# Kernel tuning notes

Measured on AMD Instinct MI355X. Metric: run time of the kernel, lower is better.

Reference implementation:

```python
import jax, jax.numpy as jnp
import numpy as np
from jax import lax

DS = 4  # downsample_factor

def setup_inputs() -> dict:
    key = jax.random.key(0)
    ks = jax.random.split(key, 7)
    B, C, H, W = 4, 256, 256, 256
    Cq = C // 16  # reduction=16
    return {
        "x":  jax.random.normal(ks[0], (B, C, H, W), dtype=jnp.float32),
        "Wq": jax.random.normal(ks[1], (Cq, C), dtype=jnp.float32) * 0.05,
        "bq": jax.random.normal(ks[2], (Cq,), dtype=jnp.float32) * 0.05,
        "Wk": jax.random.normal(ks[3], (Cq, C), dtype=jnp.float32) * 0.05,
        "bk": jax.random.normal(ks[4], (Cq,), dtype=jnp.float32) * 0.05,
        "Wv": jax.random.normal(ks[5], (C, C), dtype=jnp.float32) * 0.05,
        "bv": jax.random.normal(ks[6], (C,), dtype=jnp.float32) * 0.05,
    }

def reference(x, Wq, bq, Wk, bk, Wv, bv):
    B, C, H, W = x.shape
    # MaxPool2d(kernel=DS, stride=DS)
    xd = lax.reduce_window(x, -jnp.inf, lax.max,
                           (1, 1, DS, DS), (1, 1, DS, DS), 'VALID')
    h, w = xd.shape[2], xd.shape[3]
    N = h * w
    # 1x1 convs == channel-wise linear maps
    q = jnp.einsum('oc,bchw->bohw', Wq, xd) + bq[None, :, None, None]
    k = jnp.einsum('oc,bchw->bohw', Wk, xd) + bk[None, :, None, None]
    v = jnp.einsum('oc,bchw->bohw', Wv, xd) + bv[None, :, None, None]
    query = q.reshape(B, -1, N).transpose(0, 2, 1)   # [B, N, Cq]
    key_  = k.reshape(B, -1, N)                      # [B, Cq, N]
    value = v.reshape(B, C, N).transpose(0, 2, 1)    # [B, N, C]
    att = jnp.einsum('bnc,bcm->bnm', query, key_)    # [B, N, N]
    # global-mean threshold masking (zeros, not -inf, per original)
    att = jnp.where(att < att.mean(), 0.0, att)
    att = jax.nn.softmax(att, axis=-1)
    out = jnp.einsum('bnm,bmc->bnc', att, value)     # [B, N, C]
    out = out.transpose(0, 2, 1).reshape(B, C, h, w)
    # bilinear upsample, align_corners=False (half-pixel centers)
    out = jax.image.resize(out, (B, C, H, W), method='bilinear')
    return out + x
```

## Files before the change

kernel.cpp:

```cpp
#include <hip/hip_runtime.h>
#include <hip/hip_bf16.h>
#include <cmath>
#include <cstdint>
#include <cstddef>

typedef unsigned short u16;
typedef __attribute__((ext_vector_type(8))) __bf16 bf16x8;
typedef __attribute__((ext_vector_type(4))) float f32x4;
typedef __attribute__((ext_vector_type(8))) unsigned short us8;
typedef __attribute__((ext_vector_type(4))) unsigned short us4;

static const size_t OFF_XD32  = 0;
static const size_t OFF_QT    = 16777216;
static const size_t OFF_KT    = 17825792;
static const size_t OFF_VT    = 18874368;
static const size_t OFF_WF    = 27262976;
static const size_t OFF_SPART = 27394048;

__device__ __forceinline__ void gl2lds16(const void* gsrc, void* ldst) {
  __builtin_amdgcn_global_load_lds(
      (const __attribute__((address_space(1))) unsigned int*)gsrc,
      (__attribute__((address_space(3))) unsigned int*)ldst, 16, 0, 0);
}

__device__ __forceinline__ float hmax4(float4 v) {
  return fmaxf(fmaxf(v.x, v.y), fmaxf(v.z, v.w));
}

__global__ __launch_bounds__(256) void k_pre(const float* __restrict__ x,
                                             const float* __restrict__ Wv,
                                             float* __restrict__ xd32,
                                             u16* __restrict__ Wf) {
  const int tid = threadIdx.x;
  if (blockIdx.x < 16) {
    const int rt = blockIdx.x;
#pragma unroll
    for (int i = 0; i < 2; ++i) {
      int s = tid + i * 256;
      int ks = s >> 6, lane = s & 63;
      const float* src = Wv + (size_t)(rt * 16 + (lane & 15)) * 256u + ks * 32 + (lane >> 4) * 8;
      float4 a = *reinterpret_cast<const float4*>(src);
      float4 b = *reinterpret_cast<const float4*>(src + 4);
      us8 o;
      o[0] = __builtin_bit_cast(u16, __float2bfloat16(a.x));
      o[1] = __builtin_bit_cast(u16, __float2bfloat16(a.y));
      o[2] = __builtin_bit_cast(u16, __float2bfloat16(a.z));
      o[3] = __builtin_bit_cast(u16, __float2bfloat16(a.w));
      o[4] = __builtin_bit_cast(u16, __float2bfloat16(b.x));
      o[5] = __builtin_bit_cast(u16, __float2bfloat16(b.y));
      o[6] = __builtin_bit_cast(u16, __float2bfloat16(b.z));
      o[7] = __builtin_bit_cast(u16, __float2bfloat16(b.w));
      *reinterpret_cast<us8*>(Wf + ((size_t)((rt * 8 + ks) * 64 + lane)) * 8u) = o;
    }
  } else {
    unsigned idx = (blockIdx.x - 16) * 256u + tid;
    unsigned xo = idx & 63u;
    unsigned yo = (idx >> 6) & 63u;
    unsigned bc = idx >> 12;
    const float* base = x + (size_t)bc * 65536u + yo * 1024u + xo * 4u;
    float m = -1e30f;
#pragma unroll
    for (int dy = 0; dy < 4; ++dy) {
      float4 v = *reinterpret_cast<const float4*>(base + dy * 256);
      m = fmaxf(m, hmax4(v));
    }
    xd32[(size_t)bc * 4096u + yo * 64u + xo] = m;
  }
}

__global__ __launch_bounds__(512) void k_qkv(const float* __restrict__ xd32,
                                             const u16* __restrict__ Wf, const float* __restrict__ bv,
                                             const float* __restrict__ Wq, const float* __restrict__ bq,
                                             const float* __restrict__ Wk, const float* __restrict__ bk,
                                             float* __restrict__ qT, float* __restrict__ kT,
                                             u16* __restrict__ vT, float* __restrict__ Spart) {
  __shared__ char smem[65536];
  const int tid = threadIdx.x;

  if (blockIdx.x < 256) {
    u16 (*Bf)[8][64][8] = reinterpret_cast<u16(*)[8][64][8]>(smem);
    const int blk = blockIdx.x;
    const int b = blk >> 6, n0 = (blk & 63) * 64;
    const int w = tid >> 6, lane = tid & 63;

#pragma unroll
    for (int p = 0; p < 8; ++p) {
      int idx = p * 512 + tid;
      int k = idx >> 4, q4 = idx & 15;
      float4 v = *reinterpret_cast<const float4*>(
          xd32 + ((size_t)b * 256 + k) * 4096u + n0 + q4 * 4);
      int ks = k >> 5, kl = (k >> 3) & 3, j = k & 7;
      int ct = q4 >> 2, nb = (q4 & 3) * 4;
      Bf[ct][ks][kl * 16 + nb + 0][j] = __builtin_bit_cast(u16, __float2bfloat16(v.x));
      Bf[ct][ks][kl * 16 + nb + 1][j] = __builtin_bit_cast(u16, __float2bfloat16(v.y));
      Bf[ct][ks][kl * 16 + nb + 2][j] = __builtin_bit_cast(u16, __float2bfloat16(v.z));
      Bf[ct][ks][kl * 16 + nb + 3][j] = __builtin_bit_cast(u16, __float2bfloat16(v.w));
    }
    __syncthreads();

    f32x4 acc[2][4];
#pragma unroll
    for (int r = 0; r < 2; ++r)
#pragma unroll
      for (int ct = 0; ct < 4; ++ct) acc[r][ct] = (f32x4){0.f, 0.f, 0.f, 0.f};
    __builtin_amdgcn_s_setprio(1);
    for (int ks = 0; ks < 8; ++ks) {
      bf16x8 Bv[4];
#pragma unroll
      for (int ct = 0; ct < 4; ++ct)
        Bv[ct] = __builtin_bit_cast(bf16x8, *reinterpret_cast<const us8*>(&Bf[ct][ks][lane][0]));
#pragma unroll
      for (int r = 0; r < 2; ++r) {
        int rt = w * 2 + r;
        bf16x8 Av = __builtin_bit_cast(bf16x8,
            *reinterpret_cast<const us8*>(Wf + ((size_t)((rt * 8 + ks) * 64 + lane)) * 8u));
#pragma unroll
        for (int ct = 0; ct < 4; ++ct)
          acc[r][ct] = __builtin_amdgcn_mfma_f32_16x16x32_bf16(Av, Bv[ct], acc[r][ct], 0, 0, 0);
      }
    }
    __builtin_amdgcn_s_setprio(0);

#pragma unroll
    for (int r = 0; r < 2; ++r) {
      int row0 = (w * 2 + r) * 16 + (lane >> 4) * 4;
#pragma unroll
      for (int rr = 0; rr < 4; ++rr) {
        int c = row0 + rr;
        float bb = bv[c];
        u16* dst = vT + ((size_t)b * 256 + c) * 4096u + n0 + (lane & 15);
#pragma unroll
        for (int ct = 0; ct < 4; ++ct)
          dst[ct * 16] = __builtin_bit_cast(u16, __float2bfloat16(acc[r][ct][rr] + bb));
      }
    }
  } else {
    float (*xs)[64] = reinterpret_cast<float(*)[64]>(smem);
    const int qb = blockIdx.x - 256;
    const int b = qb >> 6, n0 = (qb & 63) * 64;
    {
      const float* src = xd32 + (size_t)b * 1048576u + n0;
#pragma unroll
      for (int i = 0; i < 8; ++i) {
        int slot = tid + i * 512;
        int c = slot >> 4, q4 = slot & 15;
        *reinterpret_cast<float4*>(&xs[c][q4 * 4]) =
            *reinterpret_cast<const float4*>(src + (size_t)c * 4096u + q4 * 4);
      }
    }
    __syncthreads();
    const int o = tid >> 4, t4 = tid & 15;
    const float* wrow = (o < 16) ? (Wq + (size_t)o * 256u) : (Wk + (size_t)(o - 16) * 256u);
    float a0 = 0.f, a1 = 0.f, a2 = 0.f, a3 = 0.f;
    for (int c = 0; c < 256; ++c) {
      float w = wrow[c];
      float4 xv = *reinterpret_cast<const float4*>(&xs[c][t4 * 4]);
      a0 = fmaf(w, xv.x, a0);
      a1 = fmaf(w, xv.y, a1);
      a2 = fmaf(w, xv.z, a2);
      a3 = fmaf(w, xv.w, a3);
    }
    float* dst = (o < 16) ? qT : kT;
    int oo = (o < 16) ? o : (o - 16);
    float bb = (o < 16) ? bq[oo] : bk[oo];
    size_t base = ((size_t)b * 4096u + n0 + t4 * 4) * 16u + oo;
    dst[base]      = a0 + bb;
    dst[base + 16] = a1 + bb;
    dst[base + 32] = a2 + bb;
    dst[base + 48] = a3 + bb;
    float s = a0 + a1 + a2 + a3;
    s += __shfl_xor(s, 1); s += __shfl_xor(s, 2);
    s += __shfl_xor(s, 4); s += __shfl_xor(s, 8);
    if (t4 == 0) Spart[(size_t)qb * 32u + o] = s;
  }
}

__global__ __launch_bounds__(512) void k_flash(const float* __restrict__ qT,
                                               const float* __restrict__ kT,
                                               const u16* __restrict__ vT,
                                               const float* __restrict__ Spart,
                                               const float* __restrict__ bq,
                                               const float* __restrict__ bk,
                                               float* __restrict__ ods) {
  __shared__ u16 vbuf[2][16384];
  __shared__ u16 kfh[2][4][64][8];
  __shared__ u16 kfl[2][4][64][8];
  __shared__ u16 pfr[8][2][64][8];
  __shared__ float mean_s;

  const int orig = blockIdx.x;
  const int b    = (orig >> 1) & 3;
  const int row0 = (((orig & 1) << 5) | (orig >> 3)) * 64;
  const int tid  = threadIdx.x;
  const int w    = tid >> 6;
  const int lane = tid & 63;
  const int wq   = w & 3;
  const int wc   = w >> 2;
  const int g    = lane >> 4;
  const int c16  = lane & 15;

  if (tid < 64) {
    int bb = tid >> 4, o = tid & 15;
    float sq = 4096.0f * bq[o], sk = 4096.0f * bk[o];
    for (int s = 0; s < 64; ++s) {
      const float* p = Spart + ((size_t)(bb * 64 + s)) * 32u;
      sq += p[o];
      sk += p[16 + o];
    }
    float pr = sq * sk;
#pragma unroll
    for (int off = 32; off > 0; off >>= 1) pr += __shfl_down(pr, off);
    if (tid == 0) mean_s = pr * (1.0f / 67108864.0f);
  }

  float qv[16];
  {
    const float* qrow = qT + ((size_t)b*4096 + row0 + 16*wq + c16) * 16;
#pragma unroll
    for (int i = 0; i < 4; ++i) {
      float4 t4 = reinterpret_cast<const float4*>(qrow)[i];
      qv[4*i] = t4.x; qv[4*i+1] = t4.y; qv[4*i+2] = t4.z; qv[4*i+3] = t4.w;
    }
  }
  u16 qhi[16], qlo[16];
#pragma unroll
  for (int i = 0; i < 16; ++i) {
    __hip_bfloat16 h = __float2bfloat16(qv[i]);
    float fh = __bfloat162float(h);
    __hip_bfloat16 lo = __float2bfloat16(qv[i] - fh);
    qhi[i] = __builtin_bit_cast(u16, h);
    qlo[i] = __builtin_bit_cast(u16, lo);
  }
  us8 a1u, a2u;
  {
    const bool koff8  = (g & 1);
    const bool lo_src = (g >= 2);
#pragma unroll
    for (int i = 0; i < 8; ++i) {
      u16 hs = koff8 ? qhi[i+8] : qhi[i];
      u16 ls = koff8 ? qlo[i+8] : qlo[i];
      a1u[i] = lo_src ? ls : hs;
      a2u[i] = lo_src ? (u16)0 : hs;
    }
  }
  const bf16x8 A1 = __builtin_bit_cast(bf16x8, a1u);
  const bf16x8 A2 = __builtin_bit_cast(bf16x8, a2u);

  f32x4 O[8];
#pragma unroll
  for (int i = 0; i < 8; ++i) O[i] = (f32x4){0.f, 0.f, 0.f, 0.f};
  float Lr[4] = {0.f, 0.f, 0.f, 0.f};
  float M = 0.0f;

  const int kv_s = tid >> 2, t4v = tid & 3;
  const int ks = kv_s >> 4, kld0 = (kv_s & 15) + 16*(t4v >> 1), ki0 = 4*(t4v & 1);

  {
    const u16* vsrc = vT + (size_t)b*256*4096;
#pragma unroll
    for (int i = 0; i < 4; ++i) {
      int u = i*512 + tid;
      int row = u >> 3, slot = u & 7;
      int sb = (slot*16) ^ ((row & 7) << 4);
      gl2lds16((const char*)(vsrc + (size_t)row*4096) + sb, (char*)&vbuf[0][0] + u*16);
    }
    if (tid < 256) {
      float4 kvec = *reinterpret_cast<const float4*>(kT + ((size_t)b*4096 + kv_s)*16 + 4*t4v);
      float kf[4] = {kvec.x, kvec.y, kvec.z, kvec.w};
      us4 h4, l4;
#pragma unroll
      for (int di = 0; di < 4; ++di) {
        __hip_bfloat16 h = __float2bfloat16(kf[di]);
        float fh = __bfloat162float(h);
        __hip_bfloat16 lo = __float2bfloat16(kf[di] - fh);
        h4[di] = __builtin_bit_cast(u16, h);
        l4[di] = __builtin_bit_cast(u16, lo);
      }
      *reinterpret_cast<us4*>(&kfh[0][ks][kld0][ki0])    = h4;
      *reinterpret_cast<us4*>(&kfh[0][ks][kld0+32][ki0]) = h4;
      *reinterpret_cast<us4*>(&kfl[0][ks][kld0][ki0])    = l4;
      *reinterpret_cast<us4*>(&kfl[0][ks][kld0+32][ki0]) = l4;
    }
  }
  __syncthreads();
  const float mean = mean_s;

  for (int t = 0; t < 64; ++t) {
    const int cur = t & 1, nxt = cur ^ 1;
    const int kv0n = ((t + 1) & 63) * 64;

    float4 kvec;
    if (tid < 256)
      kvec = *reinterpret_cast<const float4*>(kT + ((size_t)b*4096 + kv0n + kv_s)*16 + 4*t4v);
    {
      const u16* vsrc = vT + (size_t)b*256*4096 + kv0n;
#pragma unroll
      for (int i = 0; i < 4; ++i) {
        int u = i*512 + tid;
        int row = u >> 3, slot = u & 7;
        int sb = (slot*16) ^ ((row & 7) << 4);
        gl2lds16((const char*)(vsrc + (size_t)row*4096) + sb, (char*)&vbuf[nxt][0] + u*16);
      }
    }

    f32x4 S[4];
    __builtin_amdgcn_s_setprio(1);
#pragma unroll
    for (int s = 0; s < 4; ++s) {
      bf16x8 bh = __builtin_bit_cast(bf16x8, *reinterpret_cast<const us8*>(&kfh[cur][s][lane][0]));
      bf16x8 bl = __builtin_bit_cast(bf16x8, *reinterpret_cast<const us8*>(&kfl[cur][s][lane][0]));
      f32x4 acc = (f32x4){0.f, 0.f, 0.f, 0.f};
      acc = __builtin_amdgcn_mfma_f32_16x16x32_bf16(A1, bh, acc, 0, 0, 0);
      acc = __builtin_amdgcn_mfma_f32_16x16x32_bf16(A2, bl, acc, 0, 0, 0);
      S[s] = acc;
    }
    __builtin_amdgcn_s_setprio(0);

    float pmax = -1e30f;
#pragma unroll
    for (int s = 0; s < 4; ++s)
#pragma unroll
      for (int r = 0; r < 4; ++r) {
        float v = S[s][r];
        v = (v < mean) ? 0.f : v;
        S[s][r] = v;
        pmax = fmaxf(pmax, v);
      }
    if (!__all(pmax <= M + 8.0f)) {
      float mw = pmax;
#pragma unroll
      for (int off = 1; off < 64; off <<= 1) mw = fmaxf(mw, __shfl_xor(mw, off));
      float Mn = fmaxf(M, mw);
      float sc = __expf(M - Mn);
#pragma unroll
      for (int i = 0; i < 8; ++i) {
        O[i][0] *= sc; O[i][1] *= sc; O[i][2] *= sc; O[i][3] *= sc;
      }
#pragma unroll
      for (int r = 0; r < 4; ++r) Lr[r] *= sc;
      M = Mn;
    }
    u16 pb[4][4];
#pragma unroll
    for (int s = 0; s < 4; ++s)
#pragma unroll
      for (int r = 0; r < 4; ++r) {
        float p = __expf(S[s][r] - M);
        Lr[r] += p;
        pb[s][r] = __builtin_bit_cast(u16, __float2bfloat16(p));
      }

    {
      const int ib = lane & 7;
      const int t1 = (lane >> 3) & 1;
#pragma unroll
      for (int s = 0; s < 4; ++s) {
        const int c2 = s >> 1;
        const int ldb = 16 * ((2*s + t1) & 3) + 4*g;
#pragma unroll
        for (int r = 0; r < 4; ++r) pfr[w][c2][ldb + r][ib] = pb[s][r];
      }
    }
    asm volatile("s_waitcnt lgkmcnt(0)" ::: "memory");
    __builtin_amdgcn_sched_barrier(0);

    __builtin_amdgcn_s_setprio(1);
#pragma unroll
    for (int c2 = 0; c2 < 2; ++c2) {
      bf16x8 pa = __builtin_bit_cast(bf16x8, *reinterpret_cast<const us8*>(&pfr[w][c2][lane][0]));
#pragma unroll
      for (int ct = 0; ct < 8; ++ct) {
        int row = (wc*8 + ct)*16 + c16;
        int off = (c2*64 + g*16) ^ ((lane & 7) << 4);
        bf16x8 vb = __builtin_bit_cast(bf16x8,
            *reinterpret_cast<const us8*>((const char*)&vbuf[cur][0] + row*128 + off));
        O[ct] = __builtin_amdgcn_mfma_f32_16x16x32_bf16(pa, vb, O[ct], 0, 0, 0);
      }
    }
    __builtin_amdgcn_s_setprio(0);

    if (tid < 256) {
      float kf[4] = {kvec.x, kvec.y, kvec.z, kvec.w};
      us4 h4, l4;
#pragma unroll
      for (int di = 0; di < 4; ++di) {
        __hip_bfloat16 h = __float2bfloat16(kf[di]);
        float fh = __bfloat162float(h);
        __hip_bfloat16 lo = __float2bfloat16(kf[di] - fh);
        h4[di] = __builtin_bit_cast(u16, h);
        l4[di] = __builtin_bit_cast(u16, lo);
      }
      *reinterpret_cast<us4*>(&kfh[nxt][ks][kld0][ki0])    = h4;
      *reinterpret_cast<us4*>(&kfh[nxt][ks][kld0+32][ki0]) = h4;
      *reinterpret_cast<us4*>(&kfl[nxt][ks][kld0][ki0])    = l4;
      *reinterpret_cast<us4*>(&kfl[nxt][ks][kld0+32][ki0]) = l4;
    }

    __syncthreads();
  }

#pragma unroll
  for (int r = 0; r < 4; ++r) {
    float v = Lr[r];
#pragma unroll
    for (int off = 1; off < 16; off <<= 1) v += __shfl_xor(v, off);
    Lr[r] = v;
  }
  float inv[4];
#pragma unroll
  for (int r = 0; r < 4; ++r) inv[r] = 1.0f / Lr[r];
#pragma unroll
  for (int ct = 0; ct < 8; ++ct) {
    int c = (wc*8 + ct)*16 + c16;
    float* dst = ods + ((size_t)b*256 + c) * 4096u + row0 + 16*wq + 4*g;
    float4 o4 = make_float4(O[ct][0]*inv[0], O[ct][1]*inv[1], O[ct][2]*inv[2], O[ct][3]*inv[3]);
    *reinterpret_cast<float4*>(dst) = o4;
  }
}

__global__ __launch_bounds__(256) void k_up(const float* __restrict__ ods, const float* __restrict__ x,
                                            float* __restrict__ out) {
  unsigned idx4 = blockIdx.x * 256u + threadIdx.x;
  int a  = (int)(idx4 & 63u);
  int i  = (int)((idx4 >> 6) & 255u);
  size_t bc = idx4 >> 14;

  float py = (i + 0.5f) * 0.25f - 0.5f;
  float y0f = floorf(py);
  float wy = py - y0f;
  int y0 = (int)y0f, y1 = y0 + 1;
  y0 = max(y0, 0); y1 = min(y1, 63);

  int xm1 = max(a - 1, 0), xp1 = min(a + 1, 63);

  const float* r0 = ods + bc * 4096u + y0 * 64;
  const float* r1 = ods + bc * 4096u + y1 * 64;
  float wy1 = 1.f - wy;
  float vm1 = wy1 * r0[xm1] + wy * r1[xm1];
  float v0  = wy1 * r0[a]   + wy * r1[a];
  float vp1 = wy1 * r0[xp1] + wy * r1[xp1];

  float4 xv = *reinterpret_cast<const float4*>(x + (size_t)idx4 * 4u);
  float4 o4;
  o4.x = fmaf(0.375f, vm1, 0.625f * v0) + xv.x;
  o4.y = fmaf(0.125f, vm1, 0.875f * v0) + xv.y;
  o4.z = fmaf(0.875f, v0, 0.125f * vp1) + xv.z;
  o4.w = fmaf(0.625f, v0, 0.375f * vp1) + xv.w;
  *reinterpret_cast<float4*>(out + (size_t)idx4 * 4u) = o4;
}

extern "C" void kernel_launch(void* const* d_in, const int* in_sizes, int n_in,
                              void* d_out, int out_size, void* d_ws, size_t ws_size,
                              hipStream_t stream) {
  const float* x  = (const float*)d_in[0];
  const float* Wq = (const float*)d_in[1];
  const float* bq = (const float*)d_in[2];
  const float* Wk = (const float*)d_in[3];
  const float* bk = (const float*)d_in[4];
  const float* Wv = (const float*)d_in[5];
  const float* bv = (const float*)d_in[6];
  float* out = (float*)d_out;

  char* ws = (char*)d_ws;
  float* xd32  = (float*)(ws + OFF_XD32);
  float* qT    = (float*)(ws + OFF_QT);
  float* kT    = (float*)(ws + OFF_KT);
  u16*   vT    = (u16*)(ws + OFF_VT);
  u16*   Wf    = (u16*)(ws + OFF_WF);
  float* Spart = (float*)(ws + OFF_SPART);
  float* ods   = xd32;

  k_pre<<<dim3(16400), dim3(256), 0, stream>>>(x, Wv, xd32, Wf);
  k_qkv<<<dim3(512), dim3(512), 0, stream>>>(xd32, Wf, bv, Wq, bq, Wk, bk, qT, kT, vT, Spart);
  k_flash<<<dim3(256), dim3(512), 0, stream>>>(qT, kT, vT, Spart, bq, bk, ods);
  k_up<<<dim3(65536), dim3(256), 0, stream>>>(ods, x, out);
}
```

Before: 284.7 us.

## Compute attention scores once per query tile and share probabilities across warp pairs

Before this change, both warps that share a query tile (differing only in output-channel half) each computed QK scores, masking, the online-softmax rescale and exp. Now only the first four warps do that work. They publish the bf16 probability tiles and the rescale factor through LDS, and the other four warps apply the factor to their accumulators. The final row sums are shared through LDS as well. This halves the score and exp work but adds an extra block-wide barrier per KV tile and leaves half the warps idle during the softmax phase. The s_setprio hints are also removed.

After: 273.6 us. 3.9% less time.

```diff
diff --git a/kernel.cpp b/kernel.cpp
--- a/kernel.cpp
+++ b/kernel.cpp
@@ -103,7 +103,6 @@
     for (int r = 0; r < 2; ++r)
 #pragma unroll
       for (int ct = 0; ct < 4; ++ct) acc[r][ct] = (f32x4){0.f, 0.f, 0.f, 0.f};
-    __builtin_amdgcn_s_setprio(1);
     for (int ks = 0; ks < 8; ++ks) {
       bf16x8 Bv[4];
 #pragma unroll
@@ -119,7 +118,6 @@
           acc[r][ct] = __builtin_amdgcn_mfma_f32_16x16x32_bf16(Av, Bv[ct], acc[r][ct], 0, 0, 0);
       }
     }
-    __builtin_amdgcn_s_setprio(0);
 
 #pragma unroll
     for (int r = 0; r < 2; ++r) {
@@ -185,7 +183,9 @@
   __shared__ u16 vbuf[2][16384];
   __shared__ u16 kfh[2][4][64][8];
   __shared__ u16 kfl[2][4][64][8];
-  __shared__ u16 pfr[8][2][64][8];
+  __shared__ u16 pfr[4][2][64][8];
+  __shared__ float scs[4];
+  __shared__ float Ls[4][4][4];
   __shared__ float mean_s;
 
   const int orig = blockIdx.x;
@@ -198,6 +198,7 @@
   const int wc   = w >> 2;
   const int g    = lane >> 4;
   const int c16  = lane & 15;
+  const bool is_cw = (w < 4);
 
   if (tid < 64) {
     int bb = tid >> 4, o = tid & 15;
@@ -303,71 +304,83 @@
       }
     }
 
-    f32x4 S[4];
-    __builtin_amdgcn_s_setprio(1);
-#pragma unroll
-    for (int s = 0; s < 4; ++s) {
-      bf16x8 bh = __builtin_bit_cast(bf16x8, *reinterpret_cast<const us8*>(&kfh[cur][s][lane][0]));
-      bf16x8 bl = __builtin_bit_cast(bf16x8, *reinterpret_cast<const us8*>(&kfl[cur][s][lane][0]));
-      f32x4 acc = (f32x4){0.f, 0.f, 0.f, 0.f};
-      acc = __builtin_amdgcn_mfma_f32_16x16x32_bf16(A1, bh, acc, 0, 0, 0);
-      acc = __builtin_amdgcn_mfma_f32_16x16x32_bf16(A2, bl, acc, 0, 0, 0);
-      S[s] = acc;
-    }
-    __builtin_amdgcn_s_setprio(0);
-
-    float pmax = -1e30f;
-#pragma unroll
-    for (int s = 0; s < 4; ++s)
-#pragma unroll
-      for (int r = 0; r < 4; ++r) {
-        float v = S[s][r];
-        v = (v < mean) ? 0.f : v;
-        S[s][r] = v;
-        pmax = fmaxf(pmax, v);
-      }
-    if (!__all(pmax <= M + 8.0f)) {
-      float mw = pmax;
-#pragma unroll
-      for (int off = 1; off < 64; off <<= 1) mw = fmaxf(mw, __shfl_xor(mw, off));
-      float Mn = fmaxf(M, mw);
-      float sc = __expf(M - Mn);
-#pragma unroll
-      for (int i = 0; i < 8; ++i) {
-        O[i][0] *= sc; O[i][1] *= sc; O[i][2] *= sc; O[i][3] *= sc;
-      }
-#pragma unroll
-      for (int r = 0; r < 4; ++r) Lr[r] *= sc;
-      M = Mn;
-    }
-    u16 pb[4][4];
-#pragma unroll
-    for (int s = 0; s < 4; ++s)
-#pragma unroll
-      for (int r = 0; r < 4; ++r) {
-        float p = __expf(S[s][r] - M);
-        Lr[r] += p;
-        pb[s][r] = __builtin_bit_cast(u16, __float2bfloat16(p));
-      }
-
-    {
-      const int ib = lane & 7;
-      const int t1 = (lane >> 3) & 1;
+    if (is_cw) {
+      f32x4 S[4];
 #pragma unroll
       for (int s = 0; s < 4; ++s) {
-        const int c2 = s >> 1;
-        const int ldb = 16 * ((2*s + t1) & 3) + 4*g;
-#pragma unroll
-        for (int r = 0; r < 4; ++r) pfr[w][c2][ldb + r][ib] = pb[s][r];
-      }
-    }
-    asm volatile("s_waitcnt lgkmcnt(0)" ::: "memory");
-    __builtin_amdgcn_sched_barrier(0);
-
-    __builtin_amdgcn_s_setprio(1);
+        bf16x8 bh = __builtin_bit_cast(bf16x8, *reinterpret_cast<const us8*>(&kfh[cur][s][lane][0]));
+        bf16x8 bl = __builtin_bit_cast(bf16x8, *reinterpret_cast<const us8*>(&kfl[cur][s][lane][0]));
+        f32x4 acc = (f32x4){0.f, 0.f, 0.f, 0.f};
+        acc = __builtin_amdgcn_mfma_f32_16x16x32_bf16(A1, bh, acc, 0, 0, 0);
+        acc = __builtin_amdgcn_mfma_f32_16x16x32_bf16(A2, bl, acc, 0, 0, 0);
+        S[s] = acc;
+      }
+
+      float pmax = -1e30f;
+#pragma unroll
+      for (int s = 0; s < 4; ++s)
+#pragma unroll
+        for (int r = 0; r < 4; ++r) {
+          float v = S[s][r];
+          v = (v < mean) ? 0.f : v;
+          S[s][r] = v;
+          pmax = fmaxf(pmax, v);
+        }
+      float sc_out = 1.0f;
+      if (!__all(pmax <= M + 8.0f)) {
+        float mw = pmax;
+#pragma unroll
+        for (int off = 1; off < 64; off <<= 1) mw = fmaxf(mw, __shfl_xor(mw, off));
+        float Mn = fmaxf(M, mw);
+        float sc = __expf(M - Mn);
+#pragma unroll
+        for (int i = 0; i < 8; ++i) {
+          O[i][0] *= sc; O[i][1] *= sc; O[i][2] *= sc; O[i][3] *= sc;
+        }
+#pragma unroll
+        for (int r = 0; r < 4; ++r) Lr[r] *= sc;
+        M = Mn;
+        sc_out = sc;
+      }
+      if (lane == 0) scs[wq] = sc_out;
+
+      u16 pb[4][4];
+#pragma unroll
+      for (int s = 0; s < 4; ++s)
+#pragma unroll
+        for (int r = 0; r < 4; ++r) {
+          float p = __expf(S[s][r] - M);
+          Lr[r] += p;
+          pb[s][r] = __builtin_bit_cast(u16, __float2bfloat16(p));
+        }
+
+      {
+        const int ib = lane & 7;
+        const int t1 = (lane >> 3) & 1;
+#pragma unroll
+        for (int s = 0; s < 4; ++s) {
+          const int c2 = s >> 1;
+          const int ldb = 16 * ((2*s + t1) & 3) + 4*g;
+#pragma unroll
+          for (int r = 0; r < 4; ++r) pfr[wq][c2][ldb + r][ib] = pb[s][r];
+        }
+      }
+    }
+    __syncthreads();
+
+    if (!is_cw) {
+      float sc = scs[wq];
+      if (sc != 1.0f) {
+#pragma unroll
+        for (int i = 0; i < 8; ++i) {
+          O[i][0] *= sc; O[i][1] *= sc; O[i][2] *= sc; O[i][3] *= sc;
+        }
+      }
+    }
+
 #pragma unroll
     for (int c2 = 0; c2 < 2; ++c2) {
-      bf16x8 pa = __builtin_bit_cast(bf16x8, *reinterpret_cast<const us8*>(&pfr[w][c2][lane][0]));
+      bf16x8 pa = __builtin_bit_cast(bf16x8, *reinterpret_cast<const us8*>(&pfr[wq][c2][lane][0]));
 #pragma unroll
       for (int ct = 0; ct < 8; ++ct) {
         int row = (wc*8 + ct)*16 + c16;
@@ -377,7 +390,6 @@
         O[ct] = __builtin_amdgcn_mfma_f32_16x16x32_bf16(pa, vb, O[ct], 0, 0, 0);
       }
     }
-    __builtin_amdgcn_s_setprio(0);
 
     if (tid < 256) {
       float kf[4] = {kvec.x, kvec.y, kvec.z, kvec.w};
@@ -399,16 +411,28 @@
     __syncthreads();
   }
 
-#pragma unroll
-  for (int r = 0; r < 4; ++r) {
-    float v = Lr[r];
-#pragma unroll
-    for (int off = 1; off < 16; off <<= 1) v += __shfl_xor(v, off);
-    Lr[r] = v;
-  }
+  if (is_cw) {
+#pragma unroll
+    for (int r = 0; r < 4; ++r) {
+      float v = Lr[r];
+#pragma unroll
+      for (int off = 1; off < 16; off <<= 1) v += __shfl_xor(v, off);
+      Lr[r] = v;
+    }
+    if (c16 == 0) {
+#pragma unroll
+      for (int r = 0; r < 4; ++r) Ls[wq][g][r] = Lr[r];
+    }
+  }
+  __syncthreads();
   float inv[4];
-#pragma unroll
-  for (int r = 0; r < 4; ++r) inv[r] = 1.0f / Lr[r];
+  if (is_cw) {
+#pragma unroll
+    for (int r = 0; r < 4; ++r) inv[r] = 1.0f / Lr[r];
+  } else {
+#pragma unroll
+    for (int r = 0; r < 4; ++r) inv[r] = 1.0f / Ls[wq][g][r];
+  }
 #pragma unroll
   for (int ct = 0; ct < 8; ++ct) {
     int c = (wc*8 + ct)*16 + c16;
```
